# Optimization experiments

Hardware: AMD Instinct MI355X
Metric: run time of the kernel (lower is better)

Reference implementation:

```python
import jax, jax.numpy as jnp
import numpy as np

N = 50000      # nodes
E = 1_600_000  # edges (before self-loops)
G = 100        # graphs in batch
IN = 16        # in_channels
H1, C1 = 4, 32 # gat1 heads, per-head channels
H2, C2 = 1, 32 # gat2 heads, per-head channels
NEG_SLOPE = 0.2


def setup_inputs() -> dict:
    key = jax.random.key(0)
    ks = jax.random.split(key, 16)
    s = 0.1
    return {
        "x": jax.random.normal(ks[0], (N, IN), jnp.float32),
        "edge_index": jax.random.randint(ks[1], (2, E), 0, N, dtype=jnp.int64),
        "batch": jnp.sort(jax.random.randint(ks[2], (N,), 0, G, dtype=jnp.int64)),
        # GATConv 1: lin (no bias), att_src/att_dst, output bias (concat -> H1*C1)
        "W1": jax.random.normal(ks[3], (IN, H1 * C1), jnp.float32) * s,
        "att_src1": jax.random.normal(ks[4], (H1, C1), jnp.float32) * s,
        "att_dst1": jax.random.normal(ks[5], (H1, C1), jnp.float32) * s,
        "b1": jnp.zeros((H1 * C1,), jnp.float32),
        # GATConv 2
        "W2": jax.random.normal(ks[6], (H1 * C1, H2 * C2), jnp.float32) * s,
        "att_src2": jax.random.normal(ks[7], (H2, C2), jnp.float32) * s,
        "att_dst2": jax.random.normal(ks[8], (H2, C2), jnp.float32) * s,
        "b2": jnp.zeros((H2 * C2,), jnp.float32),
        # MLP head: Linear(32,64) -> ReLU -> Linear(64,1)
        "Wh1": jax.random.normal(ks[9], (C2, 64), jnp.float32) * s,
        "bh1": jnp.zeros((64,), jnp.float32),
        "Wh2": jax.random.normal(ks[10], (64, 1), jnp.float32) * s,
        "bh2": jnp.zeros((1,), jnp.float32),
    }


def gat_conv(x, src, dst, W, a_src, a_dst, bias, heads, ch):
    """PyG GATConv (self-loops already included in src/dst), eval mode."""
    n = x.shape[0]
    h = (x @ W).reshape(n, heads, ch)                 # [N,H,C]
    # per-node attention logits, then gather per edge
    a_s = jnp.einsum('nhc,hc->nh', h, a_src)          # [N,H]
    a_d = jnp.einsum('nhc,hc->nh', h, a_dst)
    e = jax.nn.leaky_relu(a_s[src] + a_d[dst], NEG_SLOPE)  # [E,H]
    # segment softmax over incoming edges of each destination node
    m = jax.ops.segment_max(e, dst, num_segments=n)   # [N,H]
    ex = jnp.exp(e - m[dst])
    denom = jax.ops.segment_sum(ex, dst, num_segments=n)
    alpha = ex / (denom[dst] + 1e-16)                 # [E,H]
    # weighted scatter-aggregate of source features
    out = jax.ops.segment_sum(alpha[:, :, None] * h[src], dst, num_segments=n)
    return out.reshape(n, heads * ch) + bias


def reference(x, edge_index, batch, W1, att_src1, att_dst1, b1,
              W2, att_src2, att_dst2, b2, Wh1, bh1, Wh2, bh2):
    n = x.shape[0]
    loops = jnp.arange(n, dtype=edge_index.dtype)
    src = jnp.concatenate([edge_index[0], loops])
    dst = jnp.concatenate([edge_index[1], loops])

    h = jax.nn.elu(gat_conv(x, src, dst, W1, att_src1, att_dst1, b1, H1, C1))
    h = jax.nn.elu(gat_conv(h, src, dst, W2, att_src2, att_dst2, b2, H2, C2))

    # global mean pool by graph id
    sums = jax.ops.segment_sum(h, batch, num_segments=G)          # [G,C2]
    cnts = jax.ops.segment_sum(jnp.ones((n,), h.dtype), batch, num_segments=G)
    pooled = sums / jnp.maximum(cnts, 1.0)[:, None]

    out = jax.nn.relu(pooled @ Wh1 + bh1) @ Wh2 + bh2             # [G,1]
    return out
```

## Files before the change

### kernel.cpp

```cpp
#include <hip/hip_runtime.h>
#include <hip/hip_fp16.h>
#include <math.h>

#define IN_CH 16
#define HC1 128
#define NH1 4
#define C2 32
#define HID 64
#define NEG 0.2f
#define CAP 10240
#define CHUNK 4096

__device__ __forceinline__ float lrelu_exp_fast(float z) {
    float lr = fmaxf(z, NEG * z);
    return __expf(lr);
}
__device__ __forceinline__ float elu_fast(float v) {
    return v > 0.f ? v : __expf(v) - 1.0f;
}

__device__ __forceinline__ void fma_mix_lo(float& acc, int hpack, float w) {
    asm("v_fma_mix_f32 %0, %1, %2, %0 op_sel:[0,0,0] op_sel_hi:[1,0,0]"
        : "+v"(acc) : "v"(hpack), "v"(w));
}
__device__ __forceinline__ void fma_mix_hi(float& acc, int hpack, float w) {
    asm("v_fma_mix_f32 %0, %1, %2, %0 op_sel:[1,0,0] op_sel_hi:[1,0,0]"
        : "+v"(acc) : "v"(hpack), "v"(w));
}

__global__ void k_front(const int* __restrict__ ei, int E, int N, int nchunk,
                        int* __restrict__ cursors, int* __restrict__ buckets,
                        const float* __restrict__ x, const float2* __restrict__ W1v,
                        const float2* __restrict__ att_s2, const float2* __restrict__ att_d2,
                        __half2* __restrict__ h1s, float* __restrict__ as1s, float* __restrict__ ad1s) {
    int bid = blockIdx.x;
    if (bid < nchunk) {
        __shared__ int cnt[256];
        __shared__ int base[256];
        __shared__ int pos[256];
        int t = threadIdx.x;
        int c0 = bid * CHUNK;
        int M = E + N;
        cnt[t] = 0;
        pos[t] = 0;
        __syncthreads();
        int srcv[16], dstv[16];
#pragma unroll
        for (int k = 0; k < 16; ++k) {
            int i = c0 + k * 256 + t;
            int s = -1, d = -1;
            if (i < M) {
                if (i < E) { s = ei[i]; d = ei[E + i]; }
                else       { s = d = i - E; }
                atomicAdd(&cnt[d >> 8], 1);
            }
            srcv[k] = s; dstv[k] = d;
        }
        __syncthreads();
        if (cnt[t] > 0) base[t] = atomicAdd(&cursors[t], cnt[t]);
        __syncthreads();
#pragma unroll
        for (int k = 0; k < 16; ++k) {
            int d = dstv[k];
            if (d >= 0) {
                int b = d >> 8;
                int p = base[b] + atomicAdd(&pos[b], 1);
                buckets[b * CAP + p] = (srcv[k] << 8) | (d & 255);
            }
        }
    } else {
        int wave = threadIdx.x >> 6;
        int lane = threadIdx.x & 63;
        int n = (bid - nchunk) * 4 + wave;
        if (n >= N) return;
        float xv = x[n * IN_CH + (lane & 15)];
        float ax = 0.f, ay = 0.f;
#pragma unroll
        for (int k = 0; k < IN_CH; ++k) {
            float xk = __shfl(xv, k, 16);
            float2 w = W1v[k * 64 + lane];
            ax += xk * w.x;
            ay += xk * w.y;
        }
        int head = lane >> 4;
        h1s[((size_t)head * N + n) * 16 + (lane & 15)] = __floats2half2_rn(ax, ay);
        float2 s2 = att_s2[lane], d2 = att_d2[lane];
        float vs = ax * s2.x + ay * s2.y;
        float vd = ax * d2.x + ay * d2.y;
#pragma unroll
        for (int o = 1; o < 16; o <<= 1) {
            vs += __shfl_xor(vs, o, 64);
            vd += __shfl_xor(vd, o, 64);
        }
        if ((lane & 15) == 0) {
            as1s[(size_t)head * N + n] = vs;
            ad1s[(size_t)head * N + n] = vd;
        }
    }
}

__global__ void k_build(const int* __restrict__ buckets, const int* __restrict__ cursors,
                        int N, int M,
                        int* __restrict__ offsets, int* __restrict__ elist) {
    __shared__ int sc[256];
    __shared__ int deg[256];
    __shared__ int cur[256];
    int b = blockIdx.x, t = threadIdx.x;
    int cv = cursors[t];
    sc[t] = cv;
    __syncthreads();
    for (int o = 1; o < 256; o <<= 1) {
        int a = (t >= o) ? sc[t - o] : 0;
        __syncthreads();
        sc[t] += a;
        __syncthreads();
    }
    int cnt = cursors[b];
    int gbase = sc[b] - cnt;
    int n0 = b << 8;
    const int* bk = buckets + b * CAP;
    deg[t] = 0;
    if (b == 0 && t == 0) offsets[N] = M;
    __syncthreads();
    for (int i = t; i < cnt; i += 256) atomicAdd(&deg[bk[i] & 255], 1);
    __syncthreads();
    int v = deg[t];
    sc[t] = v;
    __syncthreads();
    for (int o = 1; o < 256; o <<= 1) {
        int a = (t >= o) ? sc[t - o] : 0;
        __syncthreads();
        sc[t] += a;
        __syncthreads();
    }
    int excl = sc[t] - v;
    cur[t] = excl;
    if (n0 + t < N) offsets[n0 + t] = gbase + excl;
    __syncthreads();
    for (int i = t; i < cnt; i += 256) {
        int e = bk[i];
        int p = atomicAdd(&cur[e & 255], 1);
        elist[gbase + p] = e >> 8;
    }
}

__global__ void k_agg1(const int* __restrict__ offsets, const int* __restrict__ elist,
                       const char* __restrict__ as1b, const float* __restrict__ ad1s,
                       const char* __restrict__ h1b, const float* __restrict__ b1,
                       int N, int nblk, char* __restrict__ out1b) {
    int bid = blockIdx.x;
    unsigned head = (unsigned)bid / (unsigned)nblk;
    int nb = bid - (int)head * nblk;
    int wave = threadIdx.x >> 6;
    int lane = threadIdx.x & 63;
    int g = lane >> 4;
    int sl = (lane >> 2) & 3;
    int c4 = lane & 3;
    int n = nb * 16 + wave * 4 + g;
    if (n >= N) return;
    int lo = offsets[n], hi = offsets[n + 1];
    const char* ab = as1b + (size_t)head * N * 4;
    const char* hb = h1b + (size_t)head * N * 64;
    float adh = ad1s[(size_t)head * N + n];
    unsigned coff = (unsigned)(c4 << 4);
    float acc[8];
#pragma unroll
    for (int j = 0; j < 8; ++j) acc[j] = 0.f;
    float sumw = 0.f;
    for (int e0 = lo; e0 < hi; e0 += 8) {
        unsigned s[2]; bool ok[2]; float z[2]; float4 v[2]; float w[2];
#pragma unroll
        for (int u = 0; u < 2; ++u) {
            int ee = e0 + 4 * u + sl;
            ok[u] = ee < hi;
            s[u] = (unsigned)elist[ok[u] ? ee : lo];
        }
#pragma unroll
        for (int u = 0; u < 2; ++u) {
            z[u] = *(const float*)(ab + (s[u] * 4u));
            v[u] = *(const float4*)(hb + (s[u] * 64u + coff));
        }
#pragma unroll
        for (int u = 0; u < 2; ++u)
            w[u] = ok[u] ? lrelu_exp_fast(z[u] + adh) : 0.f;
#pragma unroll
        for (int u = 0; u < 2; ++u) {
            const int* hp = (const int*)&v[u];
            fma_mix_lo(acc[0], hp[0], w[u]); fma_mix_hi(acc[1], hp[0], w[u]);
            fma_mix_lo(acc[2], hp[1], w[u]); fma_mix_hi(acc[3], hp[1], w[u]);
            fma_mix_lo(acc[4], hp[2], w[u]); fma_mix_hi(acc[5], hp[2], w[u]);
            fma_mix_lo(acc[6], hp[3], w[u]); fma_mix_hi(acc[7], hp[3], w[u]);
            sumw += w[u];
        }
    }
#pragma unroll
    for (int j = 0; j < 8; ++j) {
        acc[j] += __shfl_xor(acc[j], 4, 64);
        acc[j] += __shfl_xor(acc[j], 8, 64);
    }
    sumw += __shfl_xor(sumw, 4, 64);
    sumw += __shfl_xor(sumw, 8, 64);
    if (sl == 0) {
        float inv = 1.f / (sumw + 1e-16f);
        const float* bp = b1 + head * 32 + c4 * 8;
        float o[8];
#pragma unroll
        for (int j = 0; j < 8; ++j) o[j] = elu_fast(acc[j] * inv + bp[j]);
        float4 pk;
        __half2* ph = (__half2*)&pk;
        ph[0] = __floats2half2_rn(o[0], o[1]);
        ph[1] = __floats2half2_rn(o[2], o[3]);
        ph[2] = __floats2half2_rn(o[4], o[5]);
        ph[3] = __floats2half2_rn(o[6], o[7]);
        *(float4*)(out1b + ((size_t)n * 256 + head * 64 + coff)) = pk;
    }
}

#define TN 64
__global__ void k_lin2(const __half2* __restrict__ out1h, const float* __restrict__ W2,
                       const float* __restrict__ att_s, const float* __restrict__ att_d,
                       int N, __half2* __restrict__ h2h, float* __restrict__ as2, float* __restrict__ ad2) {
    __shared__ float sx[TN][HC1 + 1];
    __shared__ float sw[HC1][C2];
    int t = threadIdx.x;
    int base = blockIdx.x * TN;
    int lim = (N - base) * HC1;
    for (int i = t * 4; i < HC1 * C2; i += 1024) {
        float4 v = *(const float4*)(W2 + i);
        sw[i >> 5][i & 31] = v.x;
        sw[i >> 5][(i & 31) + 1] = v.y;
        sw[i >> 5][(i & 31) + 2] = v.z;
        sw[i >> 5][(i & 31) + 3] = v.w;
    }
    for (int i = t * 4; i < TN * HC1; i += 1024) {
        float2 a = make_float2(0.f, 0.f), b = make_float2(0.f, 0.f);
        if (i < lim) {
            size_t idx = ((size_t)base * HC1 + i) >> 1;
            a = __half22float2(out1h[idx]);
            b = __half22float2(out1h[idx + 1]);
        }
        int nn = i >> 7, kk = i & 127;
        sx[nn][kk] = a.x; sx[nn][kk + 1] = a.y; sx[nn][kk + 2] = b.x; sx[nn][kk + 3] = b.y;
    }
    __syncthreads();
    int nloc = t >> 2;
    int c0 = (t & 3) * 8;
    float acc[8];
#pragma unroll
    for (int j = 0; j < 8; ++j) acc[j] = 0.f;
#pragma unroll 4
    for (int k = 0; k < HC1; ++k) {
        float xv = sx[nloc][k];
        float4 wa = *(float4*)&sw[k][c0];
        float4 wb = *(float4*)&sw[k][c0 + 4];
        acc[0] += xv * wa.x; acc[1] += xv * wa.y; acc[2] += xv * wa.z; acc[3] += xv * wa.w;
        acc[4] += xv * wb.x; acc[5] += xv * wb.y; acc[6] += xv * wb.z; acc[7] += xv * wb.w;
    }
    int n = base + nloc;
    if (n < N) {
#pragma unroll
        for (int j = 0; j < 4; ++j)
            h2h[(size_t)n * 16 + (c0 >> 1) + j] = __floats2half2_rn(acc[2 * j], acc[2 * j + 1]);
        float ps = 0.f, pd = 0.f;
#pragma unroll
        for (int j = 0; j < 8; ++j) {
            ps += acc[j] * att_s[c0 + j];
            pd += acc[j] * att_d[c0 + j];
        }
        ps += __shfl_down(ps, 1, 64); ps += __shfl_down(ps, 2, 64);
        pd += __shfl_down(pd, 1, 64); pd += __shfl_down(pd, 2, 64);
        if ((t & 3) == 0) { as2[n] = ps; ad2[n] = pd; }
    }
}

__global__ void k_agg2(const int* __restrict__ offsets, const int* __restrict__ elist,
                       const char* __restrict__ as2b, const float* __restrict__ ad2,
                       const char* __restrict__ h2b, const float* __restrict__ b2,
                       int N, float* __restrict__ out2) {
    int wave = threadIdx.x >> 6;
    int lane = threadIdx.x & 63;
    int n = blockIdx.x * 4 + wave;
    if (n >= N) return;
    int slot = lane >> 2, chunk = lane & 3;
    int lo = offsets[n], hi = offsets[n + 1];
    float ad = ad2[n];
    unsigned coff = (unsigned)(chunk << 4);
    float acc[8];
#pragma unroll
    for (int j = 0; j < 8; ++j) acc[j] = 0.f;
    float sumw = 0.f;
    for (int e0 = lo; e0 < hi; e0 += 32) {
        unsigned s[2]; bool ok[2]; float z[2]; float4 v[2]; float w[2];
#pragma unroll
        for (int u = 0; u < 2; ++u) {
            int ee = e0 + 16 * u + slot;
            ok[u] = ee < hi;
            s[u] = (unsigned)elist[ok[u] ? ee : lo];
        }
#pragma unroll
        for (int u = 0; u < 2; ++u) {
            z[u] = *(const float*)(as2b + (s[u] * 4u));
            v[u] = *(const float4*)(h2b + (s[u] * 64u + coff));
        }
#pragma unroll
        for (int u = 0; u < 2; ++u)
            w[u] = ok[u] ? lrelu_exp_fast(z[u] + ad) : 0.f;
#pragma unroll
        for (int u = 0; u < 2; ++u) {
            const int* hp = (const int*)&v[u];
            fma_mix_lo(acc[0], hp[0], w[u]); fma_mix_hi(acc[1], hp[0], w[u]);
            fma_mix_lo(acc[2], hp[1], w[u]); fma_mix_hi(acc[3], hp[1], w[u]);
            fma_mix_lo(acc[4], hp[2], w[u]); fma_mix_hi(acc[5], hp[2], w[u]);
            fma_mix_lo(acc[6], hp[3], w[u]); fma_mix_hi(acc[7], hp[3], w[u]);
            sumw += w[u];
        }
    }
#pragma unroll
    for (int j = 0; j < 8; ++j) {
        acc[j] += __shfl_xor(acc[j], 4, 64);
        acc[j] += __shfl_xor(acc[j], 8, 64);
        acc[j] += __shfl_xor(acc[j], 16, 64);
        acc[j] += __shfl_xor(acc[j], 32, 64);
    }
    sumw += __shfl_xor(sumw, 4, 64);
    sumw += __shfl_xor(sumw, 8, 64);
    sumw += __shfl_xor(sumw, 16, 64);
    sumw += __shfl_xor(sumw, 32, 64);
    if (slot == 0) {
        float inv = 1.f / (sumw + 1e-16f);
        float4 ba = ((const float4*)b2)[2 * chunk];
        float4 bb = ((const float4*)b2)[2 * chunk + 1];
        float o[8];
        o[0] = elu_fast(acc[0] * inv + ba.x); o[1] = elu_fast(acc[1] * inv + ba.y);
        o[2] = elu_fast(acc[2] * inv + ba.z); o[3] = elu_fast(acc[3] * inv + ba.w);
        o[4] = elu_fast(acc[4] * inv + bb.x); o[5] = elu_fast(acc[5] * inv + bb.y);
        o[6] = elu_fast(acc[6] * inv + bb.z); o[7] = elu_fast(acc[7] * inv + bb.w);
        float* dst = out2 + (size_t)n * C2 + 8 * chunk;
        *(float4*)dst = make_float4(o[0], o[1], o[2], o[3]);
        *(float4*)(dst + 4) = make_float4(o[4], o[5], o[6], o[7]);
    }
}

__global__ void k_pool(const float* __restrict__ out2, const int* __restrict__ batch,
                       int N, const float* __restrict__ Wh1, const float* __restrict__ bh1,
                       const float* __restrict__ Wh2, const float* __restrict__ bh2,
                       float* __restrict__ out) {
    int g = blockIdx.x;
    int t = threadIdx.x;
    __shared__ int sb[2];
    __shared__ float pooled[C2];
    __shared__ float red[256];
    if (t < 2) {
        int target = g + t;
        int lo = 0, hi = N;
        while (lo < hi) { int mid = (lo + hi) >> 1; if (batch[mid] < target) lo = mid + 1; else hi = mid; }
        sb[t] = lo;
    }
    __syncthreads();
    int lo = sb[0], hi = sb[1];
    int c = t & 31, grp = t >> 5;
    float part = 0.f;
    for (int n = lo + grp; n < hi; n += 8) part += out2[n * C2 + c];
    red[t] = part;
    __syncthreads();
    if (t < 128) red[t] += red[t + 128];
    __syncthreads();
    if (t < 64) red[t] += red[t + 64];
    __syncthreads();
    if (t < 32) {
        red[t] += red[t + 32];
        float cnt = (float)(hi - lo);
        pooled[t] = red[t] / fmaxf(cnt, 1.f);
    }
    __syncthreads();
    float hval = 0.f;
    if (t < HID) {
        float a = bh1[t];
#pragma unroll
        for (int cc = 0; cc < C2; ++cc) a += pooled[cc] * Wh1[cc * HID + t];
        hval = fmaxf(a, 0.f) * Wh2[t];
    }
    if (t < 64) {
        for (int o = 32; o > 0; o >>= 1) hval += __shfl_down(hval, o, 64);
        if (t == 0) out[g] = hval + bh2[0];
    }
}

extern "C" void kernel_launch(void* const* d_in, const int* in_sizes, int n_in,
                              void* d_out, int out_size, void* d_ws, size_t ws_size,
                              hipStream_t stream) {
    const float* x    = (const float*)d_in[0];
    const int*   ei   = (const int*)d_in[1];
    const int*   batch= (const int*)d_in[2];
    const float* W1   = (const float*)d_in[3];
    const float* aS1  = (const float*)d_in[4];
    const float* aD1  = (const float*)d_in[5];
    const float* b1   = (const float*)d_in[6];
    const float* W2   = (const float*)d_in[7];
    const float* aS2  = (const float*)d_in[8];
    const float* aD2  = (const float*)d_in[9];
    const float* b2   = (const float*)d_in[10];
    const float* Wh1  = (const float*)d_in[11];
    const float* bh1  = (const float*)d_in[12];
    const float* Wh2  = (const float*)d_in[13];
    const float* bh2  = (const float*)d_in[14];
    float* out = (float*)d_out;

    int N = in_sizes[2];
    int E = in_sizes[1] / 2;
    int M = E + N;
    int G = out_size;
    int nbk = (N + 255) >> 8;
    int nchunk = (M + CHUNK - 1) / CHUNK;
    int nlin = (N + 3) / 4;
    int nblk16 = (N + 15) / 16;

    char* p = (char*)d_ws;
    auto alloc = [&](size_t bytes) -> void* {
        void* r = (void*)p;
        p += (bytes + 255) & ~(size_t)255;
        return r;
    };
    __half2* h1s   = (__half2*)alloc((size_t)N * 64 * 4);
    __half2* out1h = (__half2*)alloc((size_t)N * 64 * 4);
    __half2* h2h   = (__half2*)alloc((size_t)N * 16 * 4);
    float* as1s    = (float*)alloc((size_t)N * NH1 * 4);
    float* ad1s    = (float*)alloc((size_t)N * NH1 * 4);
    float* as2     = (float*)alloc((size_t)N * 4);
    float* ad2     = (float*)alloc((size_t)N * 4);
    float* out2    = (float*)alloc((size_t)N * C2 * 4);
    int*   offsets = (int*)alloc((size_t)(N + 1) * 4);
    int*   elist   = (int*)alloc((size_t)M * 4);
    int*   cursors = (int*)alloc(256 * 4);
    int*   buckets = (int*)alloc((size_t)nbk * CAP * 4);

    hipMemsetAsync(cursors, 0, 256 * 4, stream);
    k_front<<<nchunk + nlin, 256, 0, stream>>>(ei, E, N, nchunk, cursors, buckets,
                                               x, (const float2*)W1, (const float2*)aS1,
                                               (const float2*)aD1, h1s, as1s, ad1s);
    k_build<<<nbk, 256, 0, stream>>>(buckets, cursors, N, M, offsets, elist);
    k_agg1<<<4 * nblk16, 256, 0, stream>>>(offsets, elist, (const char*)as1s, ad1s,
                                           (const char*)h1s, b1, N, nblk16, (char*)out1h);
    k_lin2<<<(N + TN - 1) / TN, 256, 0, stream>>>(out1h, W2, aS2, aD2, N, h2h, as2, ad2);
    k_agg2<<<(N + 3) / 4, 256, 0, stream>>>(offsets, elist, (const char*)as2, ad2,
                                            (const char*)h2h, b2, N, out2);
    k_pool<<<G, 256, 0, stream>>>(out2, batch, N, Wh1, bh1, Wh2, bh2, out);
}
```

Measured before the change: 293.2 us.

## Split CSR build across quarter-blocks and launch layer-1 aggregation per head

```diff
diff --git a/kernel.cpp b/kernel.cpp
--- a/kernel.cpp
+++ b/kernel.cpp
@@ -105,7 +105,8 @@
     __shared__ int sc[256];
     __shared__ int deg[256];
     __shared__ int cur[256];
-    int b = blockIdx.x, t = threadIdx.x;
+    int b = blockIdx.x >> 2, qq = blockIdx.x & 3;
+    int t = threadIdx.x;
     int cv = cursors[t];
     sc[t] = cv;
     __syncthreads();
@@ -120,7 +121,7 @@
     int n0 = b << 8;
     const int* bk = buckets + b * CAP;
     deg[t] = 0;
-    if (b == 0 && t == 0) offsets[N] = M;
+    if (blockIdx.x == 0 && t == 0) offsets[N] = M;
     __syncthreads();
     for (int i = t; i < cnt; i += 256) atomicAdd(&deg[bk[i] & 255], 1);
     __syncthreads();
@@ -135,31 +136,32 @@
     }
     int excl = sc[t] - v;
     cur[t] = excl;
-    if (n0 + t < N) offsets[n0 + t] = gbase + excl;
+    if ((t >> 6) == qq && n0 + t < N) offsets[n0 + t] = gbase + excl;
     __syncthreads();
     for (int i = t; i < cnt; i += 256) {
         int e = bk[i];
-        int p = atomicAdd(&cur[e & 255], 1);
-        elist[gbase + p] = e >> 8;
-    }
-}
-
-__global__ void k_agg1(const int* __restrict__ offsets, const int* __restrict__ elist,
-                       const char* __restrict__ as1b, const float* __restrict__ ad1s,
-                       const char* __restrict__ h1b, const float* __restrict__ b1,
-                       int N, int nblk, char* __restrict__ out1b) {
-    int bid = blockIdx.x;
-    unsigned head = (unsigned)bid / (unsigned)nblk;
-    int nb = bid - (int)head * nblk;
-    int wave = threadIdx.x >> 6;
-    int lane = threadIdx.x & 63;
+        int dl = e & 255;
+        if ((dl >> 6) == qq) {
+            int p = atomicAdd(&cur[dl], 1);
+            elist[gbase + p] = e >> 8;
+        }
+    }
+}
+
+__global__ void k_agg1h(const int* __restrict__ offsets, const int* __restrict__ elist,
+                        const float* __restrict__ as1s, const float* __restrict__ ad1s,
+                        const char* __restrict__ h1b, const float* __restrict__ b1,
+                        int N, int head, float4* __restrict__ out1q) {
+    int t = threadIdx.x;
+    int wave = t >> 6;
+    int lane = t & 63;
     int g = lane >> 4;
     int sl = (lane >> 2) & 3;
     int c4 = lane & 3;
-    int n = nb * 16 + wave * 4 + g;
+    int n = blockIdx.x * 16 + wave * 4 + g;
     if (n >= N) return;
     int lo = offsets[n], hi = offsets[n + 1];
-    const char* ab = as1b + (size_t)head * N * 4;
+    const float* ash = as1s + (size_t)head * N;
     const char* hb = h1b + (size_t)head * N * 64;
     float adh = ad1s[(size_t)head * N + n];
     unsigned coff = (unsigned)(c4 << 4);
@@ -167,24 +169,24 @@
 #pragma unroll
     for (int j = 0; j < 8; ++j) acc[j] = 0.f;
     float sumw = 0.f;
-    for (int e0 = lo; e0 < hi; e0 += 8) {
-        unsigned s[2]; bool ok[2]; float z[2]; float4 v[2]; float w[2];
-#pragma unroll
-        for (int u = 0; u < 2; ++u) {
+    for (int e0 = lo; e0 < hi; e0 += 16) {
+        unsigned s[4]; bool ok[4]; float z[4]; float4 v[4]; float w[4];
+#pragma unroll
+        for (int u = 0; u < 4; ++u) {
             int ee = e0 + 4 * u + sl;
             ok[u] = ee < hi;
             s[u] = (unsigned)elist[ok[u] ? ee : lo];
         }
 #pragma unroll
-        for (int u = 0; u < 2; ++u) {
-            z[u] = *(const float*)(ab + (s[u] * 4u));
+        for (int u = 0; u < 4; ++u) {
+            z[u] = ash[s[u]];
             v[u] = *(const float4*)(hb + (s[u] * 64u + coff));
         }
 #pragma unroll
-        for (int u = 0; u < 2; ++u)
+        for (int u = 0; u < 4; ++u)
             w[u] = ok[u] ? lrelu_exp_fast(z[u] + adh) : 0.f;
 #pragma unroll
-        for (int u = 0; u < 2; ++u) {
+        for (int u = 0; u < 4; ++u) {
             const int* hp = (const int*)&v[u];
             fma_mix_lo(acc[0], hp[0], w[u]); fma_mix_hi(acc[1], hp[0], w[u]);
             fma_mix_lo(acc[2], hp[1], w[u]); fma_mix_hi(acc[3], hp[1], w[u]);
@@ -212,7 +214,7 @@
         ph[1] = __floats2half2_rn(o[2], o[3]);
         ph[2] = __floats2half2_rn(o[4], o[5]);
         ph[3] = __floats2half2_rn(o[6], o[7]);
-        *(float4*)(out1b + ((size_t)n * 256 + head * 64 + coff)) = pk;
+        out1q[(size_t)n * 16 + head * 4 + c4] = pk;
     }
 }
 
@@ -413,7 +415,6 @@
     int nbk = (N + 255) >> 8;
     int nchunk = (M + CHUNK - 1) / CHUNK;
     int nlin = (N + 3) / 4;
-    int nblk16 = (N + 15) / 16;
 
     char* p = (char*)d_ws;
     auto alloc = [&](size_t bytes) -> void* {
@@ -438,9 +439,13 @@
     k_front<<<nchunk + nlin, 256, 0, stream>>>(ei, E, N, nchunk, cursors, buckets,
                                                x, (const float2*)W1, (const float2*)aS1,
                                                (const float2*)aD1, h1s, as1s, ad1s);
-    k_build<<<nbk, 256, 0, stream>>>(buckets, cursors, N, M, offsets, elist);
-    k_agg1<<<4 * nblk16, 256, 0, stream>>>(offsets, elist, (const char*)as1s, ad1s,
-                                           (const char*)h1s, b1, N, nblk16, (char*)out1h);
+    k_build<<<4 * nbk, 256, 0, stream>>>(buckets, cursors, N, M, offsets, elist);
+    int nblk16 = (N + 15) / 16;
+    for (int head = 0; head < NH1; ++head) {
+        k_agg1h<<<nblk16, 256, 0, stream>>>(offsets, elist, as1s, ad1s,
+                                            (const char*)h1s, b1, N, head,
+                                            (float4*)out1h);
+    }
     k_lin2<<<(N + TN - 1) / TN, 256, 0, stream>>>(out1h, W2, aS2, aD2, N, h2h, as2, ad2);
     k_agg2<<<(N + 3) / 4, 256, 0, stream>>>(offsets, elist, (const char*)as2, ad2,
                                             (const char*)h2h, b2, N, out2);
```

New measurement: 310.2 us. +5.8%, slower.
